# Optimization experiments

Measured on AMD Instinct MI355X. Metric: run time of the kernel, lower is better.

Reference implementation:

```python
import jax, jax.numpy as jnp
import numpy as np

NUM_HEADS = 16
HEAD_DIM = 64
SCALE = HEAD_DIM ** -0.5


def setup_inputs() -> dict:
    key = jax.random.key(0)
    ks = jax.random.split(key, 5)
    B, N, C = 2, 2048, 1024
    x = jax.random.normal(ks[0], (B, N, C), dtype=jnp.float32)
    rel_pos_bias = jax.random.normal(ks[1], (NUM_HEADS, N, N), dtype=jnp.float32) * 0.02
    qkv_w = jax.random.normal(ks[2], (3 * C, C), dtype=jnp.float32) * (C ** -0.5)
    q_bias = jnp.zeros((C,), dtype=jnp.float32)
    v_bias = jnp.zeros((C,), dtype=jnp.float32)
    proj_w = jax.random.normal(ks[3], (C, C), dtype=jnp.float32) * (C ** -0.5)
    proj_b = jnp.zeros((C,), dtype=jnp.float32)
    return {"x": x, "rel_pos_bias": rel_pos_bias, "qkv_w": qkv_w,
            "q_bias": q_bias, "v_bias": v_bias, "proj_w": proj_w, "proj_b": proj_b}


def reference(x, rel_pos_bias, qkv_w, q_bias, v_bias, proj_w, proj_b):
    B, N, C = x.shape
    H, D = NUM_HEADS, HEAD_DIM
    # qkv bias = concat(q_bias, zeros, v_bias)
    qkv_b = jnp.concatenate([q_bias, jnp.zeros_like(v_bias), v_bias])
    qkv = x @ qkv_w.T + qkv_b                       # [B, N, 3C]
    qkv = qkv.reshape(B, N, 3, H, D).transpose(2, 0, 3, 1, 4)  # [3, B, H, N, D]
    q, k, v = qkv[0], qkv[1], qkv[2]
    q = q * SCALE
    attn = jnp.einsum('bhnd,bhmd->bhnm', q, k)      # [B, H, N, N]
    attn = attn + rel_pos_bias[None]                # bias broadcast over batch
    attn = jax.nn.softmax(attn, axis=-1)
    out = jnp.einsum('bhnm,bhmd->bhnd', attn, v)    # [B, H, N, D]
    out = out.transpose(0, 2, 1, 3).reshape(B, N, H * D)
    out = out @ proj_w.T + proj_b
    return out
```

## Files before the change

### kernel.cpp

```cpp
#include <hip/hip_runtime.h>

typedef unsigned short u16;
typedef short bfrag __attribute__((ext_vector_type(8)));
typedef float facc  __attribute__((ext_vector_type(4)));

#define LOG2E 1.44269504088896340736f

static __device__ __forceinline__ float bf2f(u16 b) {
  union { unsigned u; float f; } v; v.u = ((unsigned)b) << 16; return v.f;
}
static __device__ __forceinline__ u16 f2bf(float x) {
  union { float f; unsigned u; } v; v.f = x;
  return (u16)((v.u + 0x7FFFu + ((v.u >> 16) & 1u)) >> 16);
}
static __device__ __forceinline__ void gload_lds16(const u16* g, u16* l) {
  __builtin_amdgcn_global_load_lds((const __attribute__((address_space(1))) void*)g,
                                   (__attribute__((address_space(3))) void*)l,
                                   16, 0, 0);
}

__global__ __launch_bounds__(256) void convert_kernel(
    const float* __restrict__ x, const float* __restrict__ qw, const float* __restrict__ pw,
    u16* __restrict__ xb, u16* __restrict__ qwb, u16* __restrict__ pwb)
{
  const int NX = 4 * 1024 * 1024, NQ = 3 * 1024 * 1024, NP = 1024 * 1024;
  const int total4 = (NX + NQ + NP) >> 2;
  for (int i = blockIdx.x * blockDim.x + threadIdx.x; i < total4;
       i += gridDim.x * blockDim.x) {
    const int e = i << 2;
    const float* s; u16* d; int off;
    if (e < NX)            { s = x;  d = xb;  off = e; }
    else if (e < NX + NQ)  { s = qw; d = qwb; off = e - NX; }
    else                   { s = pw; d = pwb; off = e - NX - NQ; }
    float4 v = *(const float4*)(s + off);
    ushort4 o;
    o.x = f2bf(v.x); o.y = f2bf(v.y); o.z = f2bf(v.z); o.w = f2bf(v.w);
    *(ushort4*)(d + off) = o;
  }
}

static __device__ __forceinline__ void gemm128_bt(
    const u16* __restrict__ A, const u16* __restrict__ B, int K,
    int m0, int n0, u16* As, u16* Bs, facc acc[4][4])
{
  const int lane = threadIdx.x & 63;
  const int wv   = threadIdx.x >> 6;
  const int quad = lane >> 4;
  const int l15  = lane & 15;
  const int wm = wv >> 1, wn = wv & 1;
  const int srow = lane >> 2;
  const int skb  = (lane & 3) * 8;

  facc zero = {0.f, 0.f, 0.f, 0.f};
#pragma unroll
  for (int i = 0; i < 4; ++i)
#pragma unroll
    for (int j = 0; j < 4; ++j) acc[i][j] = zero;

  const int nIter = K >> 5;
  for (int kk = 0; kk < nIter; ++kk) {
    const int k0 = kk << 5;
    __syncthreads();
#pragma unroll
    for (int c = 0; c < 2; ++c) {
      const int seg = wv * 2 + c;
      gload_lds16(A + (long)(m0 + seg * 16 + srow) * K + k0 + skb, As + seg * 512);
      gload_lds16(B + (long)(n0 + seg * 16 + srow) * K + k0 + skb, Bs + seg * 512);
    }
    __syncthreads();
    bfrag af[4], bf[4];
#pragma unroll
    for (int i = 0; i < 4; ++i)
      af[i] = *(const bfrag*)(As + (wm * 64 + i * 16 + l15) * 32 + quad * 8);
#pragma unroll
    for (int j = 0; j < 4; ++j)
      bf[j] = *(const bfrag*)(Bs + (wn * 64 + j * 16 + l15) * 32 + quad * 8);
#pragma unroll
    for (int i = 0; i < 4; ++i)
#pragma unroll
      for (int j = 0; j < 4; ++j)
        acc[i][j] = __builtin_amdgcn_mfma_f32_16x16x32_bf16(af[i], bf[j], acc[i][j], 0, 0, 0);
  }
}

__global__ __launch_bounds__(256) void qkv_gemm_kernel(
    const u16* __restrict__ x, const u16* __restrict__ w,
    const float* __restrict__ qb, const float* __restrict__ vb,
    u16* __restrict__ Q, u16* __restrict__ Kd, u16* __restrict__ Vt)
{
  __shared__ u16 As[128 * 32];
  __shared__ u16 Bs[128 * 32];
  facc acc[4][4];
  const int m0 = blockIdx.y * 128;
  const int n0 = blockIdx.x * 128;
  gemm128_bt(x, w, 1024, m0, n0, As, Bs, acc);

  const int lane = threadIdx.x & 63;
  const int wv = threadIdx.x >> 6;
  const int quad = lane >> 4, l15 = lane & 15;
  const int wm = wv >> 1, wn = wv & 1;
  const int ncb = n0 + wn * 64;
  const int which = ncb >> 10;
  const int h = (ncb >> 6) & 15;

#pragma unroll
  for (int j = 0; j < 4; ++j) {
    const int d = j * 16 + l15;
    const int n_g = ncb + d;
#pragma unroll
    for (int i = 0; i < 4; ++i) {
      const int mg0 = m0 + wm * 64 + i * 16 + quad * 4;
      const int b  = mg0 >> 11;
      const int ns = mg0 & 2047;
      if (which == 0) {
        const float qbv = qb[n_g];
#pragma unroll
        for (int r = 0; r < 4; ++r)
          Q[(((long)(b * 16 + h) * 2048 + ns + r) << 6) + d] =
              f2bf((acc[i][j][r] + qbv) * 0.125f);
      } else if (which == 1) {
#pragma unroll
        for (int r = 0; r < 4; ++r)
          Kd[(((long)(b * 16 + h) * 2048 + ns + r) << 6) + d] = f2bf(acc[i][j][r]);
      } else {
        const float vbv = vb[n_g - 2048];
        ushort4 pk;
        pk.x = f2bf(acc[i][j][0] + vbv);
        pk.y = f2bf(acc[i][j][1] + vbv);
        pk.z = f2bf(acc[i][j][2] + vbv);
        pk.w = f2bf(acc[i][j][3] + vbv);
        *(ushort4*)(Vt + (((long)((b * 16 + h) * 64 + d)) << 11) + ns) = pk;
      }
    }
  }
}

__global__ __launch_bounds__(256) void attn_kernel(
    const u16* __restrict__ Q, const u16* __restrict__ Kd, const u16* __restrict__ Vt,
    const float* __restrict__ bias, u16* __restrict__ AO)
{
  __shared__ u16 P[4][16 * 64];
  const int lane = threadIdx.x & 63;
  const int wv = threadIdx.x >> 6;
  const int quad = lane >> 4, l15 = lane & 15;
  const int bh = blockIdx.x >> 5;
  const int qt = blockIdx.x & 31;
  const int h = bh & 15;
  const int b = bh >> 4;
  const int q0 = qt * 64 + wv * 16;
  const long baseN = (long)bh << 17;

  bfrag qf0 = *(const bfrag*)(Q + baseN + (long)(q0 + l15) * 64 + quad * 8);
  bfrag qf1 = *(const bfrag*)(Q + baseN + (long)(q0 + l15) * 64 + 32 + quad * 8);

  facc o[4];
  float m_i[4], l_i[4];
  facc zero = {0.f, 0.f, 0.f, 0.f};
#pragma unroll
  for (int t = 0; t < 4; ++t) o[t] = zero;
#pragma unroll
  for (int r = 0; r < 4; ++r) { m_i[r] = -1e30f; l_i[r] = 0.f; }

  const float* brow = bias + ((long)h << 22) + ((long)q0 << 11);
  char* PwB = (char*)&P[wv][0];

  float bn[16];
#pragma unroll
  for (int kt = 0; kt < 4; ++kt)
#pragma unroll
    for (int r = 0; r < 4; ++r)
      bn[kt * 4 + r] =
          __builtin_nontemporal_load(brow + (long)(quad * 4 + r) * 2048 + kt * 16 + l15);

  for (int k0 = 0; k0 < 2048; k0 += 64) {
    facc s[4];
#pragma unroll
    for (int kt = 0; kt < 4; ++kt) {
      const u16* kb = Kd + baseN + (long)(k0 + kt * 16 + l15) * 64;
      bfrag kf0 = *(const bfrag*)(kb + quad * 8);
      bfrag kf1 = *(const bfrag*)(kb + 32 + quad * 8);
      facc z = zero;
      z = __builtin_amdgcn_mfma_f32_16x16x32_bf16(qf0, kf0, z, 0, 0, 0);
      z = __builtin_amdgcn_mfma_f32_16x16x32_bf16(qf1, kf1, z, 0, 0, 0);
      s[kt] = z;
    }
#pragma unroll
    for (int kt = 0; kt < 4; ++kt)
#pragma unroll
      for (int r = 0; r < 4; ++r)
        s[kt][r] += bn[kt * 4 + r];

    float alpha[4];
#pragma unroll
    for (int r = 0; r < 4; ++r) {
      float v = fmaxf(fmaxf(s[0][r], s[1][r]), fmaxf(s[2][r], s[3][r]));
      v = fmaxf(v, __shfl_xor(v, 1, 16));
      v = fmaxf(v, __shfl_xor(v, 2, 16));
      v = fmaxf(v, __shfl_xor(v, 4, 16));
      v = fmaxf(v, __shfl_xor(v, 8, 16));
      const float mn = fmaxf(m_i[r], v);
      alpha[r] = exp2f((m_i[r] - mn) * LOG2E);
      m_i[r] = mn;
    }
#pragma unroll
    for (int r = 0; r < 4; ++r) {
      const float p0 = exp2f((s[0][r] - m_i[r]) * LOG2E);
      const float p1 = exp2f((s[1][r] - m_i[r]) * LOG2E);
      const float p2 = exp2f((s[2][r] - m_i[r]) * LOG2E);
      const float p3 = exp2f((s[3][r] - m_i[r]) * LOG2E);
      s[0][r] = p0; s[1][r] = p1; s[2][r] = p2; s[3][r] = p3;
      float v = (p0 + p1) + (p2 + p3);
      v += __shfl_xor(v, 1, 16);
      v += __shfl_xor(v, 2, 16);
      v += __shfl_xor(v, 4, 16);
      v += __shfl_xor(v, 8, 16);
      l_i[r] = l_i[r] * alpha[r] + v;
    }
#pragma unroll
    for (int t = 0; t < 4; ++t)
#pragma unroll
      for (int r = 0; r < 4; ++r) o[t][r] *= alpha[r];

#pragma unroll
    for (int kt = 0; kt < 4; ++kt)
#pragma unroll
      for (int r = 0; r < 4; ++r) {
        const int row = quad * 4 + r;
        int bo = row * 128 + (kt * 16 + l15) * 2;
        bo ^= (row & 7) << 4;
        *(u16*)(PwB + bo) = f2bf(s[kt][r]);
      }

    bfrag pf[2];
#pragma unroll
    for (int p = 0; p < 2; ++p) {
      int bo = l15 * 128 + p * 64 + quad * 16;
      bo ^= (l15 & 7) << 4;
      pf[p] = *(const bfrag*)(PwB + bo);
    }

    bfrag vfr[4][2];
#pragma unroll
    for (int t = 0; t < 4; ++t) {
      const u16* vrow = Vt + baseN + (((long)(t * 16 + l15)) << 11) + k0;
#pragma unroll
      for (int p = 0; p < 2; ++p)
        vfr[t][p] = *(const bfrag*)(vrow + p * 32 + quad * 8);
    }
    if (k0 + 64 < 2048) {
      const float* bnx = brow + k0 + 64;
#pragma unroll
      for (int kt = 0; kt < 4; ++kt)
#pragma unroll
        for (int r = 0; r < 4; ++r)
          bn[kt * 4 + r] =
              __builtin_nontemporal_load(bnx + (long)(quad * 4 + r) * 2048 + kt * 16 + l15);
    }

#pragma unroll
    for (int t = 0; t < 4; ++t)
#pragma unroll
      for (int p = 0; p < 2; ++p)
        o[t] = __builtin_amdgcn_mfma_f32_16x16x32_bf16(pf[p], vfr[t][p], o[t], 0, 0, 0);
  }

#pragma unroll
  for (int r = 0; r < 4; ++r) l_i[r] = 1.0f / l_i[r];
#pragma unroll
  for (int t = 0; t < 4; ++t)
#pragma unroll
    for (int r = 0; r < 4; ++r) {
      const int row = q0 + quad * 4 + r;
      AO[(((long)(b * 2048 + row)) << 10) + h * 64 + t * 16 + l15] = f2bf(o[t][r] * l_i[r]);
    }
}

__global__ __launch_bounds__(256) void proj_kernel(
    const u16* __restrict__ Ain, const u16* __restrict__ w,
    const float* __restrict__ pb, float* __restrict__ out)
{
  __shared__ u16 As[128 * 32];
  __shared__ u16 Bs[128 * 32];
  facc acc[4][4];
  const int m0 = blockIdx.y * 128;
  const int n0 = blockIdx.x * 128;
  gemm128_bt(Ain, w, 1024, m0, n0, As, Bs, acc);

  const int lane = threadIdx.x & 63;
  const int wv = threadIdx.x >> 6;
  const int quad = lane >> 4, l15 = lane & 15;
  const int wm = wv >> 1, wn = wv & 1;
#pragma unroll
  for (int j = 0; j < 4; ++j) {
    const int n_g = n0 + wn * 64 + j * 16 + l15;
    const float pbv = pb[n_g];
#pragma unroll
    for (int i = 0; i < 4; ++i) {
      const int mg0 = m0 + wm * 64 + i * 16 + quad * 4;
#pragma unroll
      for (int r = 0; r < 4; ++r)
        out[(((long)(mg0 + r)) << 10) + n_g] = acc[i][j][r] + pbv;
    }
  }
}

extern "C" void kernel_launch(void* const* d_in, const int* in_sizes, int n_in,
                              void* d_out, int out_size, void* d_ws, size_t ws_size,
                              hipStream_t stream)
{
  const float* x    = (const float*)d_in[0];
  const float* bias = (const float*)d_in[1];
  const float* qkvw = (const float*)d_in[2];
  const float* qb   = (const float*)d_in[3];
  const float* vb   = (const float*)d_in[4];
  const float* pw   = (const float*)d_in[5];
  const float* pb   = (const float*)d_in[6];
  float* out = (float*)d_out;

  char* ws = (char*)d_ws;
  u16* Q    = (u16*)(ws);
  u16* Kd   = (u16*)(ws + (size_t)8  * 1024 * 1024);
  u16* Vt   = (u16*)(ws + (size_t)16 * 1024 * 1024);
  u16* AO   = (u16*)(ws + (size_t)24 * 1024 * 1024);
  u16* xb   = (u16*)(ws + (size_t)32 * 1024 * 1024);
  u16* qwb  = (u16*)(ws + (size_t)40 * 1024 * 1024);
  u16* pwb  = (u16*)(ws + (size_t)46 * 1024 * 1024);

  hipLaunchKernelGGL(convert_kernel, dim3(1024), dim3(256), 0, stream,
                     x, qkvw, pw, xb, qwb, pwb);
  hipLaunchKernelGGL(qkv_gemm_kernel, dim3(24, 32), dim3(256), 0, stream,
                     xb, qwb, qb, vb, Q, Kd, Vt);
  hipLaunchKernelGGL(attn_kernel, dim3(1024), dim3(256), 0, stream,
                     Q, Kd, Vt, bias, AO);
  hipLaunchKernelGGL(proj_kernel, dim3(8, 32), dim3(256), 0, stream,
                     AO, pwb, pb, out);
}
```

Baseline: 734.3 us.

## Double-buffer bias tiles in LDS via async loads and remap blocks per XCD

The attention kernel now streams each 16x64 fp32 bias tile into a per-wave, double-buffered LDS area using global_load_lds. The next tile is prefetched while the current tile is consumed, replacing the register-held nontemporal bias loads. The block index is permuted so each XCD handles a contiguous range of (batch, head, q-tile) blocks, which should improve L2 reuse of K/V. The P scratch layout is changed to a chunked format so each lane reads its MFMA fragment with one contiguous 16-byte load, V loads are interleaved with the PV MFMAs, and launch bounds request 4 blocks per CU. The trade-off is 32KB of extra LDS per block and a full vmcnt(0) wait each iteration, which may stall on outstanding K loads.

```diff
diff --git a/kernel.cpp b/kernel.cpp
--- a/kernel.cpp
+++ b/kernel.cpp
@@ -14,6 +14,11 @@
   return (u16)((v.u + 0x7FFFu + ((v.u >> 16) & 1u)) >> 16);
 }
 static __device__ __forceinline__ void gload_lds16(const u16* g, u16* l) {
+  __builtin_amdgcn_global_load_lds((const __attribute__((address_space(1))) void*)g,
+                                   (__attribute__((address_space(3))) void*)l,
+                                   16, 0, 0);
+}
+static __device__ __forceinline__ void gload_lds16f(const float* g, float* l) {
   __builtin_amdgcn_global_load_lds((const __attribute__((address_space(1))) void*)g,
                                    (__attribute__((address_space(3))) void*)l,
                                    16, 0, 0);
@@ -135,16 +140,19 @@
   }
 }
 
-__global__ __launch_bounds__(256) void attn_kernel(
+__global__ __launch_bounds__(256, 4) void attn_kernel(
     const u16* __restrict__ Q, const u16* __restrict__ Kd, const u16* __restrict__ Vt,
     const float* __restrict__ bias, u16* __restrict__ AO)
 {
   __shared__ u16 P[4][16 * 64];
+  __shared__ float BiasS[4][2][16 * 64];
   const int lane = threadIdx.x & 63;
   const int wv = threadIdx.x >> 6;
   const int quad = lane >> 4, l15 = lane & 15;
-  const int bh = blockIdx.x >> 5;
-  const int qt = blockIdx.x & 31;
+  int bid = blockIdx.x;
+  bid = (bid & 7) * 128 + (bid >> 3);
+  const int bh = bid >> 5;
+  const int qt = bid & 31;
   const int h = bh & 15;
   const int b = bh >> 4;
   const int q0 = qt * 64 + wv * 16;
@@ -163,16 +171,14 @@
 
   const float* brow = bias + ((long)h << 22) + ((long)q0 << 11);
   char* PwB = (char*)&P[wv][0];
-
-  float bn[16];
-#pragma unroll
-  for (int kt = 0; kt < 4; ++kt)
-#pragma unroll
-    for (int r = 0; r < 4; ++r)
-      bn[kt * 4 + r] =
-          __builtin_nontemporal_load(brow + (long)(quad * 4 + r) * 2048 + kt * 16 + l15);
+  float* bS[2] = { &BiasS[wv][0][0], &BiasS[wv][1][0] };
+
+#pragma unroll
+  for (int c = 0; c < 4; ++c)
+    gload_lds16f(brow + (long)(c * 4 + quad) * 2048 + l15 * 4, bS[0] + c * 256);
 
   for (int k0 = 0; k0 < 2048; k0 += 64) {
+    const float* bsCur = bS[(k0 >> 6) & 1];
     facc s[4];
 #pragma unroll
     for (int kt = 0; kt < 4; ++kt) {
@@ -184,11 +190,20 @@
       z = __builtin_amdgcn_mfma_f32_16x16x32_bf16(qf1, kf1, z, 0, 0, 0);
       s[kt] = z;
     }
+    asm volatile("s_waitcnt vmcnt(0)" ::: "memory");
 #pragma unroll
     for (int kt = 0; kt < 4; ++kt)
 #pragma unroll
       for (int r = 0; r < 4; ++r)
-        s[kt][r] += bn[kt * 4 + r];
+        s[kt][r] += bsCur[(quad * 4 + r) * 64 + kt * 16 + l15];
+
+    if (k0 + 64 < 2048) {
+      float* bsNxt = bS[((k0 >> 6) + 1) & 1];
+      const float* src = brow + k0 + 64;
+#pragma unroll
+      for (int c = 0; c < 4; ++c)
+        gload_lds16f(src + (long)(c * 4 + quad) * 2048 + l15 * 4, bsNxt + c * 256);
+    }
 
     float alpha[4];
 #pragma unroll
@@ -225,43 +240,20 @@
     for (int kt = 0; kt < 4; ++kt)
 #pragma unroll
       for (int r = 0; r < 4; ++r) {
-        const int row = quad * 4 + r;
-        int bo = row * 128 + (kt * 16 + l15) * 2;
-        bo ^= (row & 7) << 4;
+        const int bo = (kt * 2 + (l15 >> 3)) * 256 + (quad * 4 + r) * 16 + (l15 & 7) * 2;
         *(u16*)(PwB + bo) = f2bf(s[kt][r]);
       }
 
-    bfrag pf[2];
 #pragma unroll
     for (int p = 0; p < 2; ++p) {
-      int bo = l15 * 128 + p * 64 + quad * 16;
-      bo ^= (l15 & 7) << 4;
-      pf[p] = *(const bfrag*)(PwB + bo);
-    }
-
-    bfrag vfr[4][2];
-#pragma unroll
-    for (int t = 0; t < 4; ++t) {
-      const u16* vrow = Vt + baseN + (((long)(t * 16 + l15)) << 11) + k0;
-#pragma unroll
-      for (int p = 0; p < 2; ++p)
-        vfr[t][p] = *(const bfrag*)(vrow + p * 32 + quad * 8);
-    }
-    if (k0 + 64 < 2048) {
-      const float* bnx = brow + k0 + 64;
-#pragma unroll
-      for (int kt = 0; kt < 4; ++kt)
-#pragma unroll
-        for (int r = 0; r < 4; ++r)
-          bn[kt * 4 + r] =
-              __builtin_nontemporal_load(bnx + (long)(quad * 4 + r) * 2048 + kt * 16 + l15);
-    }
-
-#pragma unroll
-    for (int t = 0; t < 4; ++t)
-#pragma unroll
-      for (int p = 0; p < 2; ++p)
-        o[t] = __builtin_amdgcn_mfma_f32_16x16x32_bf16(pf[p], vfr[t][p], o[t], 0, 0, 0);
+      bfrag pfp = *(const bfrag*)(PwB + p * 1024 + lane * 16);
+#pragma unroll
+      for (int t = 0; t < 4; ++t) {
+        bfrag vf = *(const bfrag*)(Vt + baseN + (((long)(t * 16 + l15)) << 11)
+                                   + k0 + p * 32 + quad * 8);
+        o[t] = __builtin_amdgcn_mfma_f32_16x16x32_bf16(pfp, vf, o[t], 0, 0, 0);
+      }
+    }
   }
 
 #pragma unroll
```

Measured after the change: 671.8 us. 8.5% less time.
